# Optimization experiments

Hardware: AMD Instinct MI355X
Metric: run time of the kernel (lower is better)

The kernel has to match this reference:

```python
import jax, jax.numpy as jnp
import numpy as np

B, P, C = 2, 2048, 64
SIZE = 128          # image_size
K = 8               # points_per_pixel (z-buffer depth)
RADIUS = 1.5        # in pixels
RAD_POW = 2
TAU = 1.0
BIG = 1e10          # sentinel z for pixels a point does not cover


def setup_inputs() -> dict:
    key = jax.random.key(0)
    k1, k2, k3 = jax.random.split(key, 3)
    xy = jax.random.uniform(k1, (B, P, 2), minval=-1.0, maxval=1.0)   # NDC xy
    z = jax.random.uniform(k2, (B, P, 1), minval=0.1, maxval=10.0)    # depth > 0
    pts3D = jnp.concatenate([xy, z], axis=-1)                          # [B,P,3]
    src = jax.random.normal(k3, (B, C, P), dtype=jnp.float32)          # [B,C,P]
    return {"pts3D": pts3D, "src": src}


def reference(pts3D, src):
    # --- sign flips from the torch forward: pts[:, :, :2] *= -1 ---
    pts = pts3D * jnp.array([-1.0, -1.0, 1.0], dtype=pts3D.dtype)
    px, py, pz = pts[..., 0], pts[..., 1], pts[..., 2]                 # [B,P]

    r_ndc = float(RADIUS) / float(SIZE) * 2.0

    # pixel-center NDC grid (pytorch3d convention: +x left, +y up)
    ii = jnp.arange(SIZE, dtype=pts.dtype)
    ndc = 1.0 - 2.0 * (ii + 0.5) / SIZE                                # [SIZE]

    # squared NDC distance pixel->point: [B,H,W,P]
    dx = ndc[None, None, :, None] - px[:, None, None, :]               # [B,1,W,P]
    dy = ndc[None, :, None, None] - py[:, None, None, :]               # [B,H,1,P]
    d2 = dx * dx + dy * dy                                             # [B,H,W,P]

    # rasterize_points: per pixel, K nearest-in-z points within radius
    inside = d2 <= r_ndc * r_ndc
    zkey = jnp.where(inside, pz[:, None, None, :], jnp.asarray(BIG, d2.dtype))
    neg_top, idx = jax.lax.top_k(-zkey, K)            # smallest z first, [B,H,W,K]
    valid = (-neg_top) < BIG                           # idx >= 0 equivalent

    dist = jnp.take_along_axis(d2, idx, axis=-1)       # [B,H,W,K]
    dist = dist / (r_ndc ** RAD_POW)

    # alphas = (1 - clamp(dist,0.001,1)^0.5)^tau
    alphas = (1.0 - jnp.sqrt(jnp.clip(dist, 0.001, 1.0))) ** TAU
    alphas = jnp.where(valid, alphas, 0.0)

    # alpha_composite: w_k = a_k * prod_{j<k} (1 - a_j), front-to-back
    T = jnp.cumprod(1.0 - alphas, axis=-1)
    w = alphas * jnp.concatenate([jnp.ones_like(T[..., :1]), T[..., :-1]], axis=-1)

    # gather features per batch: src [B,C,P], idx [B,H,W,K] -> [B,C,H,W,K]
    gathered = jax.vmap(lambda f, i: f[:, i])(src, idx)
    out = jnp.einsum('bchwk,bhwk->bchw', gathered, w)  # [B,C,H,W]
    return out
```

## Files before the change

### kernel.cpp

```cpp
#include <hip/hip_runtime.h>

#define BATCH 2
#define NPTS 2048
#define NCH 64
#define IMG 128
#define KTOP 8
#define BIGF 1e10f
#define SEGCAP 128
#define NSEG 4

__global__ __launch_bounds__(256) void raster_mega(
    const float* __restrict__ pts,
    const float* __restrict__ src,
    float* __restrict__ out) {
  __shared__ float4 cand[NSEG][SEGCAP];
  __shared__ int scnt[NSEG];

  const int bid = blockIdx.x;
  const int half = bid & 1;
  const int h = (bid >> 1) & (IMG - 1);
  const int b = bid >> 8;
  const int t = threadIdx.x;
  const int wv = t >> 6;
  const int lane = t & 63;

  const float r_ndc = 0.0234375f;
  const float r2 = r_ndc * r_ndc;
  const float yc = 1.0f - 2.0f * (h + 0.5f) / 128.0f;

  const float* pb = pts + b * NPTS * 3;
  int base = 0;
  for (int it = 0; it < NPTS / (64 * NSEG); ++it) {
    int p = (wv << 9) + (it << 6) + lane;
    float y = pb[p * 3 + 1];
    float dy = yc + y;
    bool hit = (dy * dy <= r2);
    unsigned long long mask = __ballot(hit);
    if (mask) {
      if (hit) {
        int pos = base + __popcll(mask & ((1ull << lane) - 1ull));
        if (pos < SEGCAP)
          cand[wv][pos] = make_float4(pb[p * 3 + 0], y, pb[p * 3 + 2],
                                      __int_as_float(p));
      }
      base += __popcll(mask);
    }
  }
  if (lane == 0) scnt[wv] = min(base, SEGCAP);
  __syncthreads();

  const int w = (half << 6) + lane;
  const float xc = 1.0f - 2.0f * (w + 0.5f) / 128.0f;

  float bz[KTOP], bd[KTOP];
  int bp[KTOP];
  #pragma unroll
  for (int k = 0; k < KTOP; ++k) { bz[k] = BIGF; bd[k] = 0.f; bp[k] = 0; }

  #pragma unroll 1
  for (int seg = 0; seg < NSEG; ++seg) {
    const int cnt = scnt[seg];
    for (int j = 0; j < cnt; ++j) {
      float4 c4 = cand[seg][j];
      float dx = xc + c4.x;
      float dyy = yc + c4.y;
      float d2 = dx * dx + dyy * dyy;
      if (d2 <= r2) {
        float cz = c4.z, cd = d2;
        int cp = __float_as_int(c4.w);
        #pragma unroll
        for (int s = 0; s < KTOP; ++s) {
          bool lt = (cz < bz[s]);
          float tz = bz[s], td = bd[s];
          int tp = bp[s];
          if (lt) { bz[s] = cz; bd[s] = cd; bp[s] = cp;
                    cz = tz; cd = td; cp = tp; }
        }
      }
    }
  }

  float wgt[KTOP];
  float T = 1.0f;
  const float inv_r2 = 1.0f / r2;
  #pragma unroll
  for (int k = 0; k < KTOP; ++k) {
    float alpha = 0.0f;
    if (bz[k] < BIGF) {
      float dist = bd[k] * inv_r2;
      dist = fminf(fmaxf(dist, 0.001f), 1.0f);
      alpha = 1.0f - sqrtf(dist);
    }
    wgt[k] = alpha * T;
    T *= (1.0f - alpha);
  }

  const float* sb = src + ((size_t)b * NCH + wv * 16) * NPTS;
  float acc[16];
  #pragma unroll
  for (int c = 0; c < 16; ++c) acc[c] = 0.0f;
  #pragma unroll
  for (int k = 0; k < KTOP; ++k) {
    float wk = wgt[k];
    if (wk != 0.0f) {
      int p = bp[k];
      #pragma unroll
      for (int c = 0; c < 16; ++c)
        acc[c] += wk * sb[c * NPTS + p];
    }
  }

  float* ob = out + (((size_t)b * NCH + wv * 16) * IMG + h) * IMG + w;
  const int S = IMG * IMG;
  #pragma unroll
  for (int c = 0; c < 16; ++c)
    ob[c * S] = acc[c];
}

extern "C" void kernel_launch(void* const* d_in, const int* in_sizes, int n_in,
                              void* d_out, int out_size, void* d_ws, size_t ws_size,
                              hipStream_t stream) {
  const float* pts = (const float*)d_in[0];
  const float* src = (const float*)d_in[1];
  float* out = (float*)d_out;

  raster_mega<<<BATCH * IMG * 2, 256, 0, stream>>>(pts, src, out);
}
```

Before: 78.13 us.

## Process a full image row per block to reuse the candidate scan

Each block now handles a whole 128-pixel row: every lane evaluates two pixels (columns lane and lane+64) against the shared candidate list. The per-row y-band candidate scan of all points is done once instead of twice, and each shared-memory candidate read serves two pixels. In exchange the grid halves to 256 blocks, which may underfill the GPU's compute units, and register pressure doubles with two top-K lists and two accumulators per thread.

Result: slower. 86.00 us (+10.1%).

```diff
diff --git a/kernel.cpp b/kernel.cpp
--- a/kernel.cpp
+++ b/kernel.cpp
@@ -17,9 +17,8 @@
   __shared__ int scnt[NSEG];
 
   const int bid = blockIdx.x;
-  const int half = bid & 1;
-  const int h = (bid >> 1) & (IMG - 1);
-  const int b = bid >> 8;
+  const int h = bid & (IMG - 1);
+  const int b = bid >> 7;
   const int t = threadIdx.x;
   const int wv = t >> 6;
   const int lane = t & 63;
@@ -49,72 +48,84 @@
   if (lane == 0) scnt[wv] = min(base, SEGCAP);
   __syncthreads();
 
-  const int w = (half << 6) + lane;
-  const float xc = 1.0f - 2.0f * (w + 0.5f) / 128.0f;
+  float xc[2];
+  xc[0] = 1.0f - 2.0f * (lane + 0.5f) / 128.0f;
+  xc[1] = 1.0f - 2.0f * (lane + 64 + 0.5f) / 128.0f;
 
-  float bz[KTOP], bd[KTOP];
-  int bp[KTOP];
+  float bz[2][KTOP], bd[2][KTOP];
+  int bp[2][KTOP];
   #pragma unroll
-  for (int k = 0; k < KTOP; ++k) { bz[k] = BIGF; bd[k] = 0.f; bp[k] = 0; }
+  for (int q = 0; q < 2; ++q)
+    #pragma unroll
+    for (int k = 0; k < KTOP; ++k) { bz[q][k] = BIGF; bd[q][k] = 0.f; bp[q][k] = 0; }
 
   #pragma unroll 1
   for (int seg = 0; seg < NSEG; ++seg) {
     const int cnt = scnt[seg];
     for (int j = 0; j < cnt; ++j) {
       float4 c4 = cand[seg][j];
-      float dx = xc + c4.x;
       float dyy = yc + c4.y;
-      float d2 = dx * dx + dyy * dyy;
-      if (d2 <= r2) {
-        float cz = c4.z, cd = d2;
-        int cp = __float_as_int(c4.w);
-        #pragma unroll
-        for (int s = 0; s < KTOP; ++s) {
-          bool lt = (cz < bz[s]);
-          float tz = bz[s], td = bd[s];
-          int tp = bp[s];
-          if (lt) { bz[s] = cz; bd[s] = cd; bp[s] = cp;
-                    cz = tz; cd = td; cp = tp; }
+      #pragma unroll
+      for (int q = 0; q < 2; ++q) {
+        float dx = xc[q] + c4.x;
+        float d2 = dx * dx + dyy * dyy;
+        if (d2 <= r2) {
+          float cz = c4.z, cd = d2;
+          int cp = __float_as_int(c4.w);
+          #pragma unroll
+          for (int s = 0; s < KTOP; ++s) {
+            bool lt = (cz < bz[q][s]);
+            float tz = bz[q][s], td = bd[q][s];
+            int tp = bp[q][s];
+            if (lt) { bz[q][s] = cz; bd[q][s] = cd; bp[q][s] = cp;
+                      cz = tz; cd = td; cp = tp; }
+          }
         }
       }
     }
   }
 
-  float wgt[KTOP];
-  float T = 1.0f;
+  float wgt[2][KTOP];
   const float inv_r2 = 1.0f / r2;
   #pragma unroll
-  for (int k = 0; k < KTOP; ++k) {
-    float alpha = 0.0f;
-    if (bz[k] < BIGF) {
-      float dist = bd[k] * inv_r2;
-      dist = fminf(fmaxf(dist, 0.001f), 1.0f);
-      alpha = 1.0f - sqrtf(dist);
+  for (int q = 0; q < 2; ++q) {
+    float T = 1.0f;
+    #pragma unroll
+    for (int k = 0; k < KTOP; ++k) {
+      float alpha = 0.0f;
+      if (bz[q][k] < BIGF) {
+        float dist = bd[q][k] * inv_r2;
+        dist = fminf(fmaxf(dist, 0.001f), 1.0f);
+        alpha = 1.0f - sqrtf(dist);
+      }
+      wgt[q][k] = alpha * T;
+      T *= (1.0f - alpha);
     }
-    wgt[k] = alpha * T;
-    T *= (1.0f - alpha);
   }
 
   const float* sb = src + ((size_t)b * NCH + wv * 16) * NPTS;
-  float acc[16];
-  #pragma unroll
-  for (int c = 0; c < 16; ++c) acc[c] = 0.0f;
-  #pragma unroll
-  for (int k = 0; k < KTOP; ++k) {
-    float wk = wgt[k];
-    if (wk != 0.0f) {
-      int p = bp[k];
-      #pragma unroll
-      for (int c = 0; c < 16; ++c)
-        acc[c] += wk * sb[c * NPTS + p];
-    }
-  }
-
-  float* ob = out + (((size_t)b * NCH + wv * 16) * IMG + h) * IMG + w;
+  float* ob = out + (((size_t)b * NCH + wv * 16) * IMG + h) * IMG;
   const int S = IMG * IMG;
   #pragma unroll
-  for (int c = 0; c < 16; ++c)
-    ob[c * S] = acc[c];
+  for (int q = 0; q < 2; ++q) {
+    float acc[16];
+    #pragma unroll
+    for (int c = 0; c < 16; ++c) acc[c] = 0.0f;
+    #pragma unroll
+    for (int k = 0; k < KTOP; ++k) {
+      float wk = wgt[q][k];
+      if (wk != 0.0f) {
+        int p = bp[q][k];
+        #pragma unroll
+        for (int c = 0; c < 16; ++c)
+          acc[c] += wk * sb[c * NPTS + p];
+      }
+    }
+    const int w = (q << 6) + lane;
+    #pragma unroll
+    for (int c = 0; c < 16; ++c)
+      ob[c * S + w] = acc[c];
+  }
 }
 
 extern "C" void kernel_launch(void* const* d_in, const int* in_sizes, int n_in,
@@ -124,5 +135,5 @@
   const float* src = (const float*)d_in[1];
   float* out = (float*)d_out;
 
-  raster_mega<<<BATCH * IMG * 2, 256, 0, stream>>>(pts, src, out);
+  raster_mega<<<BATCH * IMG, 256, 0, stream>>>(pts, src, out);
 }
```
